# Kernel tuning notes

Hardware: AMD Instinct MI355X
Metric: run time of the kernel (lower is better)

Reference implementation:

```python
import jax, jax.numpy as jnp
import numpy as np

K = 16          # nodes_num
BN_EPS = 1e-5


def _bn_conv_relu(x, w, gamma, beta, mean, var):
    # 1x1 conv on [N,K,C] node features == matmul, then eval-mode BN + ReLU
    y = jnp.einsum('nkc,oc->nko', x, w)                      # [N,K,256]
    y = (y - mean) * jax.lax.rsqrt(var + BN_EPS) * gamma + beta
    return jax.nn.relu(y)


def _lnorm(r, c):
    # Symmetric-normalized affinity from node pixel coordinates.
    # A_ij = 1/(1+||p_i-p_j||), self-loops A_ii=1, Lnorm = D^-1/2 A D^-1/2
    p = jnp.stack([r, c], axis=-1).astype(jnp.float32)        # [N,K,2]
    diff = p[:, :, None, :] - p[:, None, :, :]
    dist = jnp.sqrt(jnp.sum(diff * diff, axis=-1))            # [N,K,K]
    A = 1.0 / (1.0 + dist)
    dinv = jax.lax.rsqrt(jnp.sum(A, axis=-1))                 # [N,K]
    return A * dinv[:, :, None] * dinv[:, None, :]


def setup_inputs() -> dict:
    key = jax.random.key(0)
    ks = jax.random.split(key, 12)
    N, C, W, H = 128, 1024, 14, 14
    O = 256
    inp = {
        'fpam_output': jax.random.normal(ks[0], (N, C, W, H), jnp.float32),
        'resnet_output': jax.random.normal(ks[1], (N, 2048), jnp.float32),
        'w_max': jax.random.normal(ks[2], (O, C), jnp.float32) * 0.02,
        'g_max': 1.0 + 0.1 * jax.random.normal(ks[3], (O,), jnp.float32),
        'b_max': 0.1 * jax.random.normal(ks[4], (O,), jnp.float32),
        'm_max': 0.1 * jax.random.normal(ks[5], (O,), jnp.float32),
        'v_max': jax.random.uniform(ks[6], (O,), jnp.float32, 0.5, 1.5),
        'w_med': jax.random.normal(ks[7], (O, C), jnp.float32) * 0.02,
        'g_med': 1.0 + 0.1 * jax.random.normal(ks[8], (O,), jnp.float32),
        'b_med': 0.1 * jax.random.normal(ks[9], (O,), jnp.float32),
        'm_med': 0.1 * jax.random.normal(ks[10], (O,), jnp.float32),
        'v_med': jax.random.uniform(ks[11], (O,), jnp.float32, 0.5, 1.5),
    }
    return inp


def reference(fpam_output, resnet_output, w_max, g_max, b_max, m_max, v_max,
              w_med, g_med, b_med, m_med, v_med):
    N, C, W, H = fpam_output.shape
    HW = W * H
    # channel-sum saliency, sort descending
    fre = jnp.sum(fpam_output, axis=1).reshape(N, HW)         # [N,HW]
    idx = jnp.argsort(-fre, axis=1)
    maxK = idx[:, :K]
    mstart = HW // 2 - K // 2 - 1
    medK = idx[:, mstart:mstart + K]
    scene = jnp.concatenate([maxK, medK], axis=1)             # [N,2K]
    rows = scene // H
    cols = scene % H
    # batched gather replacing the per-pixel python loop
    flat = fpam_output.reshape(N, C, HW)
    nodes = jnp.take_along_axis(flat, scene[:, None, :], axis=2)  # [N,C,2K]
    nodes = jnp.transpose(nodes, (0, 2, 1))                   # [N,2K,C]
    x_max = _bn_conv_relu(nodes[:, :K], w_max, g_max, b_max, m_max, v_max)
    x_med = _bn_conv_relu(nodes[:, K:], w_med, g_med, b_med, m_med, v_med)
    Ltop = _lnorm(rows[:, :K], cols[:, :K])
    Lmed = _lnorm(rows[:, K:], cols[:, K:])
    max_graph = jnp.einsum('nij,njc->nic', Ltop, x_max).reshape(N, -1)
    med_graph = jnp.einsum('nij,njc->nic', Lmed, x_med).reshape(N, -1)
    return (max_graph, med_graph, rows, cols)
```

## Files before the change

kernel.cpp:

```cpp
#include <hip/hip_runtime.h>

#define NB 128
#define CC 1024
#define HWP 196
#define HH 14
#define OO 256

typedef unsigned short ushort_t;
typedef __attribute__((ext_vector_type(8))) short short8;
typedef __attribute__((ext_vector_type(4))) float float4v;

__device__ __forceinline__ ushort_t f2bf(float v) {
  union { float f; unsigned int u; } c; c.f = v;
  unsigned int u = c.u;
  unsigned int r = (u + 0x7FFFu + ((u >> 16) & 1u)) >> 16;
  return (ushort_t)r;
}

__global__ __launch_bounds__(256) void k_prep(const float* __restrict__ x,
                                              const float* __restrict__ wmax,
                                              const float* __restrict__ wmed,
                                              float* __restrict__ partial,
                                              ushort_t* __restrict__ wb) {
  const int b = blockIdx.x, t = threadIdx.x;
  if (b >= 256) {
    int idx = (b - 256) * 256 + t;
    int z = idx >> 18;
    int r = idx & (OO * CC - 1);
    const float* w = z ? wmed : wmax;
    wb[idx] = f2bf(w[r]);
    return;
  }
  const int unit = b * 4 + (t >> 6);
  const int lane = t & 63;
  if (lane >= 49) return;
  const int n = unit >> 3, cg = unit & 7;
  const float4* base = (const float4*)(x + ((size_t)n * CC + (size_t)cg * 128) * HWP);
  float4 s = {0.f, 0.f, 0.f, 0.f};
  #pragma unroll 16
  for (int c = 0; c < 128; ++c) {
    float4 v = base[c * 49 + lane];
    s.x += v.x; s.y += v.y; s.z += v.z; s.w += v.w;
  }
  ((float4*)(partial + ((size_t)n * 8 + cg) * HWP))[lane] = s;
}

__global__ __launch_bounds__(512, 2) void k_main(
    const float* __restrict__ x, const float* __restrict__ partial,
    const ushort_t* __restrict__ wb,
    const float* __restrict__ g_max, const float* __restrict__ b_max,
    const float* __restrict__ m_max, const float* __restrict__ v_max,
    const float* __restrict__ g_med, const float* __restrict__ b_med,
    const float* __restrict__ m_med, const float* __restrict__ v_med,
    float* __restrict__ out) {
  constexpr int AP = 1032;
  __shared__ alignas(16) ushort_t A_sh[16 * AP];
  __shared__ float fre[HWP];
  __shared__ int sc[32];
  __shared__ float Lsh[16][17];
  __shared__ float dinv[16];
  __shared__ float y_sh[16][257];

  const int n = blockIdx.x;
  const int z = blockIdx.y;
  const int t = threadIdx.x;

  if (t < HWP) {
    float s = 0.f;
    #pragma unroll
    for (int g = 0; g < 8; ++g) s += partial[((size_t)n * 8 + g) * HWP + t];
    fre[t] = s;
  }
  __syncthreads();
  if (t < HWP) {
    float v = fre[t];
    int rank = 0;
    #pragma unroll 4
    for (int q = 0; q < HWP; ++q) {
      float u = fre[q];
      rank += ((u > v) || (u == v && q < t)) ? 1 : 0;
    }
    if (rank < 16) sc[rank] = t;
    else if (rank >= 89 && rank < 105) sc[rank - 73] = t;
  }
  __syncthreads();

  if (z == 0 && t < 32) {
    int p = sc[t];
    out[2 * NB * 4096 + n * 32 + t] = (float)(p / HH);
    out[2 * NB * 4096 + NB * 32 + n * 32 + t] = (float)(p % HH);
  }

  {
    const int j = t & 15;
    const int g = t >> 4;
    const int sj = sc[z * 16 + j];
    const float* xb = x + (size_t)n * (CC * HWP) + (size_t)g * 32 * HWP + sj;
    ushort_t* arow = &A_sh[j * AP + g * 32];
    #pragma unroll 16
    for (int u = 0; u < 32; ++u) {
      arow[u] = f2bf(xb[(size_t)u * HWP]);
    }
  }
  if (t < 256) {
    const int i = t >> 4, j = t & 15;
    int pi = sc[z * 16 + i], pj = sc[z * 16 + j];
    float dr = (float)(pi / HH - pj / HH);
    float dc = (float)(pi % HH - pj % HH);
    Lsh[i][j] = 1.0f / (1.0f + sqrtf(dr * dr + dc * dc));
  }
  __syncthreads();
  if (t < 16) {
    float s = 0.f;
    #pragma unroll
    for (int j = 0; j < 16; ++j) s += Lsh[t][j];
    dinv[t] = rsqrtf(s);
  }

  const int w = t >> 6;
  const int l = t & 63;
  const int m = l & 15;
  const int quad = l >> 4;

  const ushort_t* Arow = &A_sh[m * AP + quad * 8];
  const ushort_t* B0 = wb + (size_t)z * (OO * CC) + (size_t)(w * 32 + m) * CC + quad * 8;

  float4v acc0 = {0.f, 0.f, 0.f, 0.f};
  float4v acc1 = acc0;

  __syncthreads();

  #pragma unroll 4
  for (int k0 = 0; k0 < CC; k0 += 32) {
    short8 a  = *reinterpret_cast<const short8*>(Arow + k0);
    short8 b0 = *reinterpret_cast<const short8*>(B0 + k0);
    short8 b1 = *reinterpret_cast<const short8*>(B0 + 16 * CC + k0);
    acc0 = __builtin_amdgcn_mfma_f32_16x16x32_bf16(a, b0, acc0, 0, 0, 0);
    acc1 = __builtin_amdgcn_mfma_f32_16x16x32_bf16(a, b1, acc1, 0, 0, 0);
  }

  const float* gp = z ? g_med : g_max;
  const float* bp = z ? b_med : b_max;
  const float* mp = z ? m_med : m_max;
  const float* vp = z ? v_med : v_max;

  #pragma unroll
  for (int tt = 0; tt < 2; ++tt) {
    float4v av = tt ? acc1 : acc0;
    int o = w * 32 + tt * 16 + m;
    float scale = gp[o] * rsqrtf(vp[o] + 1e-5f);
    float shift = bp[o] - mp[o] * scale;
    #pragma unroll
    for (int r = 0; r < 4; ++r) {
      int j = quad * 4 + r;
      float y = av[r] * scale + shift;
      y = fmaxf(y, 0.f);
      y_sh[j][o] = y * dinv[j];
    }
  }
  __syncthreads();

  {
    const int o = t & 255;
    const int ih = (t >> 8) * 8;
    float yp[16];
    #pragma unroll
    for (int j = 0; j < 16; ++j) yp[j] = y_sh[j][o];
    float* ob = out + (size_t)z * (NB * 4096) + (size_t)n * 4096 + o;
    #pragma unroll
    for (int i2 = 0; i2 < 8; ++i2) {
      const int i = ih + i2;
      float s = 0.f;
      #pragma unroll
      for (int j = 0; j < 16; ++j) s = fmaf(Lsh[i][j], yp[j], s);
      ob[(size_t)i * OO] = s * dinv[i];
    }
  }
}

extern "C" void kernel_launch(void* const* d_in, const int* in_sizes, int n_in,
                              void* d_out, int out_size, void* d_ws, size_t ws_size,
                              hipStream_t stream) {
  const float* x     = (const float*)d_in[0];
  const float* w_max = (const float*)d_in[2];
  const float* g_max = (const float*)d_in[3];
  const float* b_max = (const float*)d_in[4];
  const float* m_max = (const float*)d_in[5];
  const float* v_max = (const float*)d_in[6];
  const float* w_med = (const float*)d_in[7];
  const float* g_med = (const float*)d_in[8];
  const float* b_med = (const float*)d_in[9];
  const float* m_med = (const float*)d_in[10];
  const float* v_med = (const float*)d_in[11];
  float* out = (float*)d_out;

  float* ws_f = (float*)d_ws;
  float* partial  = ws_f;
  ushort_t* wb    = (ushort_t*)(ws_f + 200704);

  k_prep<<<dim3(256 + 2048), 256, 0, stream>>>(x, w_max, w_med, partial, wb);
  k_main<<<dim3(NB, 2), 512, 0, stream>>>(x, partial, wb,
                                          g_max, b_max, m_max, v_max,
                                          g_med, b_med, m_med, v_med, out);
}
```

Measured before the change: 210.4 us.

## Pre-transpose input to pixel-major bf16 so node gather reads contiguous rows

The prep kernel now also writes a transposed bf16 copy of the full feature map (pixel-major, channels contiguous). The main kernel gathers each selected node's 1024 channels as vectorized 16-byte loads instead of strided scalar reads across channels. Prep blocks are regrouped per batch item so the reduction, transpose and weight-conversion work are interleaved. The cost is an extra full pass that writes about 51 MB of bf16 data, in exchange for removing the main kernel's uncoalesced gather.

```diff
diff --git a/kernel.cpp b/kernel.cpp
--- a/kernel.cpp
+++ b/kernel.cpp
@@ -21,33 +21,60 @@
                                               const float* __restrict__ wmax,
                                               const float* __restrict__ wmed,
                                               float* __restrict__ partial,
-                                              ushort_t* __restrict__ wb) {
-  const int b = blockIdx.x, t = threadIdx.x;
-  if (b >= 256) {
-    int idx = (b - 256) * 256 + t;
+                                              ushort_t* __restrict__ wb,
+                                              ushort_t* __restrict__ xt) {
+  const int bid = blockIdx.x, t = threadIdx.x;
+  const int n = bid / 26, r = bid % 26;
+
+  if (r >= 10) {
+    int idx = (n * 16 + (r - 10)) * 256 + t;
     int z = idx >> 18;
-    int r = idx & (OO * CC - 1);
+    int rr = idx & (OO * CC - 1);
     const float* w = z ? wmed : wmax;
-    wb[idx] = f2bf(w[r]);
+    wb[idx] = f2bf(w[rr]);
     return;
   }
-  const int unit = b * 4 + (t >> 6);
+
+  if (r >= 2) {
+    const int cg = r - 2;
+    const int pl = t & 15;
+    const int ch = t >> 4;
+    const float* xb = x + ((size_t)n * CC + cg * 128 + ch * 8) * HWP;
+    ushort_t* xo = xt + (size_t)n * HWP * CC + cg * 128 + ch * 8;
+    #pragma unroll 2
+    for (int it = 0; it <= 12; ++it) {
+      const int p = pl + 16 * it;
+      if (p < HWP) {
+        float v[8];
+        #pragma unroll
+        for (int j = 0; j < 8; ++j) v[j] = xb[(size_t)j * HWP + p];
+        short8 o;
+        #pragma unroll
+        for (int j = 0; j < 8; ++j) o[j] = (short)f2bf(v[j]);
+        *(short8*)(xo + (size_t)p * CC) = o;
+      }
+    }
+    return;
+  }
+
+  const int unit = (n * 2 + r) * 4 + (t >> 6);
   const int lane = t & 63;
   if (lane >= 49) return;
-  const int n = unit >> 3, cg = unit & 7;
-  const float4* base = (const float4*)(x + ((size_t)n * CC + (size_t)cg * 128) * HWP);
+  const int nn = unit >> 3, cg = unit & 7;
+  const float4* base = (const float4*)(x + ((size_t)nn * CC + (size_t)cg * 128) * HWP);
   float4 s = {0.f, 0.f, 0.f, 0.f};
   #pragma unroll 16
   for (int c = 0; c < 128; ++c) {
     float4 v = base[c * 49 + lane];
     s.x += v.x; s.y += v.y; s.z += v.z; s.w += v.w;
   }
-  ((float4*)(partial + ((size_t)n * 8 + cg) * HWP))[lane] = s;
+  ((float4*)(partial + ((size_t)nn * 8 + cg) * HWP))[lane] = s;
 }
 
 __global__ __launch_bounds__(512, 2) void k_main(
-    const float* __restrict__ x, const float* __restrict__ partial,
+    const float* __restrict__ partial,
     const ushort_t* __restrict__ wb,
+    const ushort_t* __restrict__ xt,
     const float* __restrict__ g_max, const float* __restrict__ b_max,
     const float* __restrict__ m_max, const float* __restrict__ v_max,
     const float* __restrict__ g_med, const float* __restrict__ b_med,
@@ -92,15 +119,13 @@
   }
 
   {
-    const int j = t & 15;
-    const int g = t >> 4;
-    const int sj = sc[z * 16 + j];
-    const float* xb = x + (size_t)n * (CC * HWP) + (size_t)g * 32 * HWP + sj;
-    ushort_t* arow = &A_sh[j * AP + g * 32];
-    #pragma unroll 16
-    for (int u = 0; u < 32; ++u) {
-      arow[u] = f2bf(xb[(size_t)u * HWP]);
-    }
+    const int j = t >> 5;
+    const int u = t & 31;
+    const ushort_t* src = xt + ((size_t)n * HWP + sc[z * 16 + j]) * CC + u * 8;
+    ushort_t* dst = &A_sh[j * AP + u * 8];
+    #pragma unroll
+    for (int q = 0; q < 4; ++q)
+      *(short8*)(dst + q * 256) = *(const short8*)(src + q * 256);
   }
   if (t < 256) {
     const int i = t >> 4, j = t & 15;
@@ -197,9 +222,10 @@
   float* ws_f = (float*)d_ws;
   float* partial  = ws_f;
   ushort_t* wb    = (ushort_t*)(ws_f + 200704);
-
-  k_prep<<<dim3(256 + 2048), 256, 0, stream>>>(x, w_max, w_med, partial, wb);
-  k_main<<<dim3(NB, 2), 512, 0, stream>>>(x, partial, wb,
+  ushort_t* xt    = wb + 2 * OO * CC;
+
+  k_prep<<<dim3(26 * NB), 256, 0, stream>>>(x, w_max, w_med, partial, wb, xt);
+  k_main<<<dim3(NB, 2), 512, 0, stream>>>(partial, wb, xt,
                                           g_max, b_max, m_max, v_max,
                                           g_med, b_med, m_med, v_med, out);
 }
```

New measurement: 236.5 us. 1.12x slower.

## Move node gather into separate extraction kernel with coalesced row reads

Applied to the files above, without the earlier changes.

Adds a k_extract kernel, spread over 1024 blocks, that recomputes the top/median ranking and gathers the selected pixel columns into a compact bf16 node matrix. It reads whole channel rows coalesced through shared memory instead of doing strided scalar loads. k_main then loads its A tile with vector loads from this compact buffer instead of doing scattered gathers from the input across only 256 blocks. The cost is an extra launch, the ranking computed twice, and rereading the full input tensor (about 100MB) a second time.

```diff
diff --git a/kernel.cpp b/kernel.cpp
--- a/kernel.cpp
+++ b/kernel.cpp
@@ -7,6 +7,7 @@
 #define OO 256
 
 typedef unsigned short ushort_t;
+typedef __attribute__((ext_vector_type(4))) short short4v;
 typedef __attribute__((ext_vector_type(8))) short short8;
 typedef __attribute__((ext_vector_type(4))) float float4v;
 
@@ -35,7 +36,7 @@
   const int lane = t & 63;
   if (lane >= 49) return;
   const int n = unit >> 3, cg = unit & 7;
-  const float4* base = (const float4*)(x + ((size_t)n * CC + (size_t)cg * 128) * HWP);
+  const float4 * base = (const float4*)(x + ((size_t)n * CC + (size_t)cg * 128) * HWP);
   float4 s = {0.f, 0.f, 0.f, 0.f};
   #pragma unroll 16
   for (int c = 0; c < 128; ++c) {
@@ -45,9 +46,66 @@
   ((float4*)(partial + ((size_t)n * 8 + cg) * HWP))[lane] = s;
 }
 
+__global__ __launch_bounds__(256) void k_extract(const float* __restrict__ x,
+                                                 const float* __restrict__ partial,
+                                                 ushort_t* __restrict__ af) {
+  __shared__ float fre[HWP];
+  __shared__ int sc[32];
+  __shared__ float rowbuf[4][200];
+  __shared__ ushort_t outbuf[4][32][36];
+
+  const int b = blockIdx.x;
+  const int n = b >> 3, cg = b & 7;
+  const int t = threadIdx.x;
+
+  if (t < HWP) {
+    float s = 0.f;
+    #pragma unroll
+    for (int g = 0; g < 8; ++g) s += partial[((size_t)n * 8 + g) * HWP + t];
+    fre[t] = s;
+  }
+  __syncthreads();
+  if (t < HWP) {
+    float v = fre[t];
+    int rank = 0;
+    #pragma unroll 4
+    for (int q = 0; q < HWP; ++q) {
+      float u = fre[q];
+      rank += ((u > v) || (u == v && q < t)) ? 1 : 0;
+    }
+    if (rank < 16) sc[rank] = t;
+    else if (rank >= 89 && rank < 105) sc[rank - 73] = t;
+  }
+  __syncthreads();
+
+  const int w = t >> 6, lane = t & 63;
+  const int c0 = cg * 128 + w * 32;
+  const float* xrow = x + ((size_t)n * CC + c0) * HWP;
+  const int sp = (lane < 32) ? sc[lane] : 0;
+
+  float4 nxt = {0.f, 0.f, 0.f, 0.f};
+  if (lane < 49) nxt = *(const float4*)(xrow + (size_t)lane * 4);
+  for (int r = 0; r < 32; ++r) {
+    float4 cur = nxt;
+    if (r < 31 && lane < 49)
+      nxt = *(const float4*)(xrow + (size_t)(r + 1) * HWP + (size_t)lane * 4);
+    if (lane < 49) *(float4*)&rowbuf[w][lane * 4] = cur;
+    if (lane < 32) outbuf[w][lane][r] = f2bf(rowbuf[w][sp]);
+  }
+  {
+    const int j = lane & 31, half = lane >> 5;
+    ushort_t* dst = af + ((size_t)n * 32 + j) * CC + c0 + half * 16;
+    const ushort_t* srcp = &outbuf[w][j][half * 16];
+    #pragma unroll
+    for (int q = 0; q < 4; ++q)
+      *(short4v*)(dst + q * 4) = *(const short4v*)(srcp + q * 4);
+  }
+}
+
 __global__ __launch_bounds__(512, 2) void k_main(
-    const float* __restrict__ x, const float* __restrict__ partial,
+    const float* __restrict__ partial,
     const ushort_t* __restrict__ wb,
+    const ushort_t* __restrict__ af,
     const float* __restrict__ g_max, const float* __restrict__ b_max,
     const float* __restrict__ m_max, const float* __restrict__ v_max,
     const float* __restrict__ g_med, const float* __restrict__ b_med,
@@ -92,15 +150,13 @@
   }
 
   {
-    const int j = t & 15;
-    const int g = t >> 4;
-    const int sj = sc[z * 16 + j];
-    const float* xb = x + (size_t)n * (CC * HWP) + (size_t)g * 32 * HWP + sj;
-    ushort_t* arow = &A_sh[j * AP + g * 32];
-    #pragma unroll 16
-    for (int u = 0; u < 32; ++u) {
-      arow[u] = f2bf(xb[(size_t)u * HWP]);
-    }
+    const int j = t >> 5;
+    const int u = t & 31;
+    const ushort_t* src = af + ((size_t)n * 32 + z * 16 + j) * CC + u * 8;
+    ushort_t* dst = &A_sh[j * AP + u * 8];
+    #pragma unroll
+    for (int q = 0; q < 4; ++q)
+      *(short8*)(dst + q * 256) = *(const short8*)(src + q * 256);
   }
   if (t < 256) {
     const int i = t >> 4, j = t & 15;
@@ -197,9 +253,11 @@
   float* ws_f = (float*)d_ws;
   float* partial  = ws_f;
   ushort_t* wb    = (ushort_t*)(ws_f + 200704);
+  ushort_t* af    = wb + 2 * OO * CC;
 
   k_prep<<<dim3(256 + 2048), 256, 0, stream>>>(x, w_max, w_med, partial, wb);
-  k_main<<<dim3(NB, 2), 512, 0, stream>>>(x, partial, wb,
+  k_extract<<<dim3(NB * 8), 256, 0, stream>>>(x, partial, af);
+  k_main<<<dim3(NB, 2), 512, 0, stream>>>(partial, wb, af,
                                           g_max, b_max, m_max, v_max,
                                           g_med, b_med, m_med, v_med, out);
 }
```

After: 221.9 us. 1.05x slower.

## Merge max/med blocks into one 1024-thread block per sample, batch gather loads

Applied to the files above, without the earlier changes.

Each sample now runs in a single 1024-thread block that handles both the max and median node groups, so the partial-sum reduction and the rank sort over 196 pixels run once per sample instead of twice. The node gather is split into two phases: 32 global loads go into registers first, the affinity matrix is built while they are in flight, and the values are then converted to bf16 and written to shared memory. The cost is half as many blocks (128 on a large GPU), more shared memory and register pressure per block, and lower occupancy.

```diff
diff --git a/kernel.cpp b/kernel.cpp
--- a/kernel.cpp
+++ b/kernel.cpp
@@ -45,7 +45,7 @@
   ((float4*)(partial + ((size_t)n * 8 + cg) * HWP))[lane] = s;
 }
 
-__global__ __launch_bounds__(512, 2) void k_main(
+__global__ __launch_bounds__(1024, 1) void k_main(
     const float* __restrict__ x, const float* __restrict__ partial,
     const ushort_t* __restrict__ wb,
     const float* __restrict__ g_max, const float* __restrict__ b_max,
@@ -54,15 +54,14 @@
     const float* __restrict__ m_med, const float* __restrict__ v_med,
     float* __restrict__ out) {
   constexpr int AP = 1032;
-  __shared__ alignas(16) ushort_t A_sh[16 * AP];
+  __shared__ alignas(16) ushort_t A_sh[32 * AP];
   __shared__ float fre[HWP];
   __shared__ int sc[32];
-  __shared__ float Lsh[16][17];
-  __shared__ float dinv[16];
-  __shared__ float y_sh[16][257];
+  __shared__ float Lsh[32][17];
+  __shared__ float dinv[32];
+  __shared__ float y_sh[32][257];
 
   const int n = blockIdx.x;
-  const int z = blockIdx.y;
   const int t = threadIdx.x;
 
   if (t < HWP) {
@@ -85,50 +84,52 @@
   }
   __syncthreads();
 
-  if (z == 0 && t < 32) {
+  if (t < 32) {
     int p = sc[t];
     out[2 * NB * 4096 + n * 32 + t] = (float)(p / HH);
     out[2 * NB * 4096 + NB * 32 + n * 32 + t] = (float)(p % HH);
   }
 
-  {
-    const int j = t & 15;
-    const int g = t >> 4;
-    const int sj = sc[z * 16 + j];
-    const float* xb = x + (size_t)n * (CC * HWP) + (size_t)g * 32 * HWP + sj;
-    ushort_t* arow = &A_sh[j * AP + g * 32];
-    #pragma unroll 16
-    for (int u = 0; u < 32; ++u) {
-      arow[u] = f2bf(xb[(size_t)u * HWP]);
-    }
-  }
-  if (t < 256) {
-    const int i = t >> 4, j = t & 15;
-    int pi = sc[z * 16 + i], pj = sc[z * 16 + j];
+  const int gj = t & 31, gg = t >> 5;
+  const int sp = sc[gj];
+  const float* gsrc = x + ((size_t)n * CC + gg * 32) * HWP + sp;
+  float gv[32];
+  #pragma unroll
+  for (int u = 0; u < 32; ++u) gv[u] = gsrc[(size_t)u * HWP];
+
+  if (t < 512) {
+    const int z2 = t >> 8, i = (t >> 4) & 15, j = t & 15;
+    int pi = sc[z2 * 16 + i], pj = sc[z2 * 16 + j];
     float dr = (float)(pi / HH - pj / HH);
     float dc = (float)(pi % HH - pj % HH);
-    Lsh[i][j] = 1.0f / (1.0f + sqrtf(dr * dr + dc * dc));
-  }
-  __syncthreads();
-  if (t < 16) {
+    Lsh[z2 * 16 + i][j] = 1.0f / (1.0f + sqrtf(dr * dr + dc * dc));
+  }
+  __syncthreads();
+  if (t < 32) {
     float s = 0.f;
     #pragma unroll
     for (int j = 0; j < 16; ++j) s += Lsh[t][j];
     dinv[t] = rsqrtf(s);
   }
+
+  {
+    ushort_t* arow = &A_sh[gj * AP + gg * 32];
+    #pragma unroll
+    for (int u = 0; u < 32; ++u) arow[u] = f2bf(gv[u]);
+  }
+  __syncthreads();
 
   const int w = t >> 6;
   const int l = t & 63;
   const int m = l & 15;
   const int quad = l >> 4;
-
-  const ushort_t* Arow = &A_sh[m * AP + quad * 8];
-  const ushort_t* B0 = wb + (size_t)z * (OO * CC) + (size_t)(w * 32 + m) * CC + quad * 8;
+  const int zz = w >> 3, wc = w & 7;
+
+  const ushort_t* Arow = &A_sh[(zz * 16 + m) * AP + quad * 8];
+  const ushort_t* B0 = wb + (size_t)zz * (OO * CC) + (size_t)(wc * 32 + m) * CC + quad * 8;
 
   float4v acc0 = {0.f, 0.f, 0.f, 0.f};
   float4v acc1 = acc0;
-
-  __syncthreads();
 
   #pragma unroll 4
   for (int k0 = 0; k0 < CC; k0 += 32) {
@@ -139,41 +140,42 @@
     acc1 = __builtin_amdgcn_mfma_f32_16x16x32_bf16(a, b1, acc1, 0, 0, 0);
   }
 
-  const float* gp = z ? g_med : g_max;
-  const float* bp = z ? b_med : b_max;
-  const float* mp = z ? m_med : m_max;
-  const float* vp = z ? v_med : v_max;
+  const float* gp = zz ? g_med : g_max;
+  const float* bp = zz ? b_med : b_max;
+  const float* mp = zz ? m_med : m_max;
+  const float* vp = zz ? v_med : v_max;
 
   #pragma unroll
   for (int tt = 0; tt < 2; ++tt) {
     float4v av = tt ? acc1 : acc0;
-    int o = w * 32 + tt * 16 + m;
+    int o = wc * 32 + tt * 16 + m;
     float scale = gp[o] * rsqrtf(vp[o] + 1e-5f);
     float shift = bp[o] - mp[o] * scale;
     #pragma unroll
     for (int r = 0; r < 4; ++r) {
-      int j = quad * 4 + r;
+      int jl = quad * 4 + r;
       float y = av[r] * scale + shift;
       y = fmaxf(y, 0.f);
-      y_sh[j][o] = y * dinv[j];
+      y_sh[zz * 16 + jl][o] = y * dinv[zz * 16 + jl];
     }
   }
   __syncthreads();
 
   {
     const int o = t & 255;
-    const int ih = (t >> 8) * 8;
+    const int gi = t >> 8;
+    const int z2 = gi >> 1;
     float yp[16];
     #pragma unroll
-    for (int j = 0; j < 16; ++j) yp[j] = y_sh[j][o];
-    float* ob = out + (size_t)z * (NB * 4096) + (size_t)n * 4096 + o;
+    for (int j = 0; j < 16; ++j) yp[j] = y_sh[z2 * 16 + j][o];
+    float* ob = out + (size_t)z2 * (NB * 4096) + (size_t)n * 4096 + o;
     #pragma unroll
     for (int i2 = 0; i2 < 8; ++i2) {
-      const int i = ih + i2;
+      const int i = (gi & 1) * 8 + i2;
       float s = 0.f;
       #pragma unroll
-      for (int j = 0; j < 16; ++j) s = fmaf(Lsh[i][j], yp[j], s);
-      ob[(size_t)i * OO] = s * dinv[i];
+      for (int j = 0; j < 16; ++j) s = fmaf(Lsh[z2 * 16 + i][j], yp[j], s);
+      ob[(size_t)i * OO] = s * dinv[z2 * 16 + i];
     }
   }
 }
@@ -199,7 +201,7 @@
   ushort_t* wb    = (ushort_t*)(ws_f + 200704);
 
   k_prep<<<dim3(256 + 2048), 256, 0, stream>>>(x, w_max, w_med, partial, wb);
-  k_main<<<dim3(NB, 2), 512, 0, stream>>>(x, partial, wb,
-                                          g_max, b_max, m_max, v_max,
-                                          g_med, b_med, m_med, v_med, out);
-}
+  k_main<<<dim3(NB), 1024, 0, stream>>>(x, partial, wb,
+                                        g_max, b_max, m_max, v_max,
+                                        g_med, b_med, m_med, v_med, out);
+}
```

Measured after the change: 221.9 us. 5.5% more time.
